# Optimization experiments

Hardware: AMD Instinct MI355X
Metric: run time of the kernel (lower is better)

Reference implementation:

```python
import jax, jax.numpy as jnp
import numpy as np

N_NODES = 50000
N_EDGES = 300000
D = 256


def setup_inputs() -> dict:
    key = jax.random.key(0)
    k1, k2, k3, k4, k5 = jax.random.split(key, 5)
    edge_feat = jax.random.normal(k1, (N_EDGES, D), dtype=jnp.float32)
    node_feat = jax.random.normal(k2, (N_NODES, D), dtype=jnp.float32)
    src_idx = jax.random.randint(k3, (N_EDGES,), 0, N_NODES, dtype=jnp.int32)
    tgt_idx = jax.random.randint(k4, (N_EDGES,), 0, N_NODES, dtype=jnp.int32)
    W = jax.random.normal(k5, (3 * D, D), dtype=jnp.float32) * (1.0 / np.sqrt(3 * D))
    b = jnp.zeros((D,), dtype=jnp.float32)
    return {"edge_feat": edge_feat, "node_feat": node_feat,
            "src_idx": src_idx, "tgt_idx": tgt_idx, "W": W, "b": b}


def reference(edge_feat, node_feat, src_idx, tgt_idx, W, b):
    # broadcast_node_to_edges: gather node states for SOURCE and TARGET tags
    src = jnp.take(node_feat, src_idx, axis=0)   # [E, D]
    tgt = jnp.take(node_feat, tgt_idx, axis=0)   # [E, D]
    # NextStateFromConcat: concat edge input + node inputs, then Dense+relu
    x = jnp.concatenate([edge_feat, src, tgt], axis=-1)  # [E, 3D]
    return jax.nn.relu(x @ W + b)                        # [E, D]
```

## Files before the change

kernel.cpp:

```cpp
#include <hip/hip_runtime.h>
#include <hip/hip_bf16.h>

typedef __attribute__((ext_vector_type(8))) short short8;
typedef __attribute__((ext_vector_type(4))) float floatx4;

#define D_DIM 256
#define K_DIM 768
#define TILE 128
#define APAD 40

__device__ __forceinline__ short f2bf(float x) {
    union { float f; unsigned u; } a; a.f = x;
    unsigned r = a.u + 0x7fffu + ((a.u >> 16) & 1u);
    return (short)(r >> 16);
}

__global__ __launch_bounds__(256) void wt_kernel(const float* __restrict__ W,
                                                 short* __restrict__ Wt) {
    __shared__ float tile[32][33];
    const int k0 = blockIdx.x * 32, n0 = blockIdx.y * 32;
    const int tx = threadIdx.x & 31, ty = threadIdx.x >> 5;
#pragma unroll
    for (int i = 0; i < 32; i += 8)
        tile[ty + i][tx] = W[(size_t)(k0 + ty + i) * D_DIM + n0 + tx];
    __syncthreads();
#pragma unroll
    for (int i = 0; i < 32; i += 8)
        Wt[(size_t)(n0 + ty + i) * K_DIM + k0 + tx] = f2bf(tile[tx][ty + i]);
}

__global__ __launch_bounds__(256, 3) void edge_gemm(
    const float* __restrict__ edge, const float* __restrict__ node,
    const int* __restrict__ src, const int* __restrict__ tgt,
    const short* __restrict__ Wt, const float* __restrict__ bias,
    float* __restrict__ out, int E)
{
    __shared__ short As[TILE][APAD];
    __shared__ short Bs[TILE][APAD];
    __shared__ int sidx[TILE], tidx[TILE];

    const int tid = threadIdx.x;
    const int m0 = blockIdx.y * TILE;
    const int n0 = blockIdx.x * TILE;

    if (tid < TILE) {
        int r = m0 + tid; if (r >= E) r = E - 1;
        sidx[tid] = src[r];
        tidx[tid] = tgt[r];
    }
    __syncthreads();

    const int srow = tid >> 1;
    const int half = tid & 1;
    int rs = m0 + srow; if (rs >= E) rs = E - 1;
    const float* ab0 = edge + (size_t)rs * D_DIM + half * 16;
    const float* ab1 = node + (size_t)sidx[srow] * D_DIM + half * 16;
    const float* ab2 = node + (size_t)tidx[srow] * D_DIM + half * 16;
    const short* wb  = Wt + (size_t)(n0 + srow) * K_DIM + half * 16;
    short* aw = &As[srow][half * 16];
    short* bw = &Bs[srow][half * 16];

    const int lane = tid & 63;
    const int wm = ((tid >> 7) & 1) * 64;
    const int wn = ((tid >> 6) & 1) * 64;
    const int fr = lane & 15;
    const int kq = (lane >> 4) * 8;

    floatx4 acc[4][4] = {};

    const float* abases[3] = { ab0, ab1, ab2 };

#pragma unroll
    for (int seg = 0; seg < 3; ++seg) {
        const float* ab = abases[seg];
        const short* wbs = wb + seg * D_DIM;
        for (int it = 0; it < 8; ++it) {
            const float4* ap = (const float4*)(ab + it * 32);
            float4 f0 = ap[0], f1 = ap[1], f2 = ap[2], f3 = ap[3];
            const short8* wp = (const short8*)(wbs + it * 32);
            short8 w0 = wp[0], w1 = wp[1];

            __syncthreads();

            union { short8 v; short s[8]; } u0, u1;
            u0.s[0] = f2bf(f0.x); u0.s[1] = f2bf(f0.y); u0.s[2] = f2bf(f0.z); u0.s[3] = f2bf(f0.w);
            u0.s[4] = f2bf(f1.x); u0.s[5] = f2bf(f1.y); u0.s[6] = f2bf(f1.z); u0.s[7] = f2bf(f1.w);
            u1.s[0] = f2bf(f2.x); u1.s[1] = f2bf(f2.y); u1.s[2] = f2bf(f2.z); u1.s[3] = f2bf(f2.w);
            u1.s[4] = f2bf(f3.x); u1.s[5] = f2bf(f3.y); u1.s[6] = f2bf(f3.z); u1.s[7] = f2bf(f3.w);
            *(short8*)aw = u0.v;       *((short8*)aw + 1) = u1.v;
            *(short8*)bw = w0;         *((short8*)bw + 1) = w1;

            __syncthreads();

            short8 afr[4], bfr[4];
#pragma unroll
            for (int i = 0; i < 4; ++i) afr[i] = *(const short8*)&As[wm + i * 16 + fr][kq];
#pragma unroll
            for (int j = 0; j < 4; ++j) bfr[j] = *(const short8*)&Bs[wn + j * 16 + fr][kq];
#pragma unroll
            for (int i = 0; i < 4; ++i)
#pragma unroll
                for (int j = 0; j < 4; ++j)
                    acc[i][j] = __builtin_amdgcn_mfma_f32_16x16x32_bf16(
                        afr[i], bfr[j], acc[i][j], 0, 0, 0);
        }
    }

    float bv[4];
#pragma unroll
    for (int j = 0; j < 4; ++j) bv[j] = bias[n0 + wn + j * 16 + fr];
    const int rq = (lane >> 4) * 4;
#pragma unroll
    for (int i = 0; i < 4; ++i) {
        const int rbase = m0 + wm + i * 16 + rq;
#pragma unroll
        for (int j = 0; j < 4; ++j) {
            const int c = n0 + wn + j * 16 + fr;
#pragma unroll
            for (int r = 0; r < 4; ++r) {
                const int rr = rbase + r;
                if (rr < E) {
                    float v = acc[i][j][r] + bv[j];
                    out[(size_t)rr * D_DIM + c] = v > 0.f ? v : 0.f;
                }
            }
        }
    }
}

extern "C" void kernel_launch(void* const* d_in, const int* in_sizes, int n_in,
                              void* d_out, int out_size, void* d_ws, size_t ws_size,
                              hipStream_t stream) {
    const float* edge = (const float*)d_in[0];
    const float* node = (const float*)d_in[1];
    const int*   srcI = (const int*)d_in[2];
    const int*   tgtI = (const int*)d_in[3];
    const float* W    = (const float*)d_in[4];
    const float* bias = (const float*)d_in[5];
    float* out = (float*)d_out;
    const int E = in_sizes[2];
    short* Wt = (short*)d_ws;

    dim3 tgrid(K_DIM / 32, D_DIM / 32);
    wt_kernel<<<tgrid, dim3(256), 0, stream>>>(W, Wt);

    dim3 ggrid(D_DIM / TILE, (E + TILE - 1) / TILE);
    edge_gemm<<<ggrid, dim3(256), 0, stream>>>(edge, node, srcI, tgtI, Wt, bias, out, E);
}
```

Before: 786.8 us.

## Load MFMA fragments directly from global memory, removing LDS staging and barriers

Each wave now loads its A and B MFMA fragments straight from global memory into registers, converting fp32 to bf16 per fragment, so the shared-memory tiles and both __syncthreads per k-step are gone. Gather pointers for the edge, source and target rows are computed per fragment row up front, and the k loop is fully unrolled. The cost is redundant global traffic: every A row is loaded by both column waves and every B row by both row waves, and each fp32 value is converted to bf16 twice. Register pressure also rises now that the occupancy hint of 3 is dropped from the launch bounds.

```diff
diff --git a/kernel.cpp b/kernel.cpp
--- a/kernel.cpp
+++ b/kernel.cpp
@@ -7,7 +7,6 @@
 #define D_DIM 256
 #define K_DIM 768
 #define TILE 128
-#define APAD 40
 
 __device__ __forceinline__ short f2bf(float x) {
     union { float f; unsigned u; } a; a.f = x;
@@ -29,74 +28,61 @@
         Wt[(size_t)(n0 + ty + i) * K_DIM + k0 + tx] = f2bf(tile[tx][ty + i]);
 }
 
-__global__ __launch_bounds__(256, 3) void edge_gemm(
+__global__ __launch_bounds__(256) void edge_gemm(
     const float* __restrict__ edge, const float* __restrict__ node,
     const int* __restrict__ src, const int* __restrict__ tgt,
     const short* __restrict__ Wt, const float* __restrict__ bias,
     float* __restrict__ out, int E)
 {
-    __shared__ short As[TILE][APAD];
-    __shared__ short Bs[TILE][APAD];
-    __shared__ int sidx[TILE], tidx[TILE];
+    const int tid  = threadIdx.x;
+    const int lane = tid & 63;
+    const int wave = tid >> 6;
+    const int wm   = (wave >> 1) * 64;
+    const int wn   = (wave & 1) * 64;
+    const int fr   = lane & 15;
+    const int kq   = (lane >> 4) * 8;
 
-    const int tid = threadIdx.x;
     const int m0 = blockIdx.y * TILE;
     const int n0 = blockIdx.x * TILE;
 
-    if (tid < TILE) {
-        int r = m0 + tid; if (r >= E) r = E - 1;
-        sidx[tid] = src[r];
-        tidx[tid] = tgt[r];
+    const float* aptr[3][4];
+#pragma unroll
+    for (int i = 0; i < 4; ++i) {
+        int r = m0 + wm + i * 16 + fr;
+        int rc = r < E ? r : E - 1;
+        int s = src[rc], t = tgt[rc];
+        aptr[0][i] = edge + (size_t)rc * D_DIM + kq;
+        aptr[1][i] = node + (size_t)s  * D_DIM + kq;
+        aptr[2][i] = node + (size_t)t  * D_DIM + kq;
     }
-    __syncthreads();
-
-    const int srow = tid >> 1;
-    const int half = tid & 1;
-    int rs = m0 + srow; if (rs >= E) rs = E - 1;
-    const float* ab0 = edge + (size_t)rs * D_DIM + half * 16;
-    const float* ab1 = node + (size_t)sidx[srow] * D_DIM + half * 16;
-    const float* ab2 = node + (size_t)tidx[srow] * D_DIM + half * 16;
-    const short* wb  = Wt + (size_t)(n0 + srow) * K_DIM + half * 16;
-    short* aw = &As[srow][half * 16];
-    short* bw = &Bs[srow][half * 16];
-
-    const int lane = tid & 63;
-    const int wm = ((tid >> 7) & 1) * 64;
-    const int wn = ((tid >> 6) & 1) * 64;
-    const int fr = lane & 15;
-    const int kq = (lane >> 4) * 8;
+    const short* bptr[4];
+#pragma unroll
+    for (int j = 0; j < 4; ++j)
+        bptr[j] = Wt + (size_t)(n0 + wn + j * 16 + fr) * K_DIM + kq;
 
     floatx4 acc[4][4] = {};
 
-    const float* abases[3] = { ab0, ab1, ab2 };
-
 #pragma unroll
     for (int seg = 0; seg < 3; ++seg) {
-        const float* ab = abases[seg];
-        const short* wbs = wb + seg * D_DIM;
+#pragma unroll
         for (int it = 0; it < 8; ++it) {
-            const float4* ap = (const float4*)(ab + it * 32);
-            float4 f0 = ap[0], f1 = ap[1], f2 = ap[2], f3 = ap[3];
-            const short8* wp = (const short8*)(wbs + it * 32);
-            short8 w0 = wp[0], w1 = wp[1];
+            short8 bfr[4];
+#pragma unroll
+            for (int j = 0; j < 4; ++j)
+                bfr[j] = *(const short8*)(bptr[j] + seg * D_DIM + it * 32);
 
-            __syncthreads();
-
-            union { short8 v; short s[8]; } u0, u1;
-            u0.s[0] = f2bf(f0.x); u0.s[1] = f2bf(f0.y); u0.s[2] = f2bf(f0.z); u0.s[3] = f2bf(f0.w);
-            u0.s[4] = f2bf(f1.x); u0.s[5] = f2bf(f1.y); u0.s[6] = f2bf(f1.z); u0.s[7] = f2bf(f1.w);
-            u1.s[0] = f2bf(f2.x); u1.s[1] = f2bf(f2.y); u1.s[2] = f2bf(f2.z); u1.s[3] = f2bf(f2.w);
-            u1.s[4] = f2bf(f3.x); u1.s[5] = f2bf(f3.y); u1.s[6] = f2bf(f3.z); u1.s[7] = f2bf(f3.w);
-            *(short8*)aw = u0.v;       *((short8*)aw + 1) = u1.v;
-            *(short8*)bw = w0;         *((short8*)bw + 1) = w1;
-
-            __syncthreads();
-
-            short8 afr[4], bfr[4];
+            short8 afr[4];
 #pragma unroll
-            for (int i = 0; i < 4; ++i) afr[i] = *(const short8*)&As[wm + i * 16 + fr][kq];
-#pragma unroll
-            for (int j = 0; j < 4; ++j) bfr[j] = *(const short8*)&Bs[wn + j * 16 + fr][kq];
+            for (int i = 0; i < 4; ++i) {
+                const float4* p = (const float4*)(aptr[seg][i] + it * 32);
+                float4 f0 = p[0], f1 = p[1];
+                union { short8 v; short s[8]; } u;
+                u.s[0] = f2bf(f0.x); u.s[1] = f2bf(f0.y);
+                u.s[2] = f2bf(f0.z); u.s[3] = f2bf(f0.w);
+                u.s[4] = f2bf(f1.x); u.s[5] = f2bf(f1.y);
+                u.s[6] = f2bf(f1.z); u.s[7] = f2bf(f1.w);
+                afr[i] = u.v;
+            }
 #pragma unroll
             for (int i = 0; i < 4; ++i)
 #pragma unroll
```

Measured after the change: 1.134 ms. 44.2% more time.
